# Optimization experiments

Measured on AMD Instinct MI355X. Metric: run time of the kernel, lower is better.

## Reference

```python
import jax, jax.numpy as jnp
import numpy as np

D = 1024
H = 16

def setup_inputs() -> dict:
    key = jax.random.key(0)
    ks = jax.random.split(key, 5)
    x = jax.random.normal(ks[0], (2, 2048, D), dtype=jnp.float32)
    s = 0.02
    W_attn = jax.random.normal(ks[1], (D, 3 * D), dtype=jnp.float32) * s
    b_attn = jnp.zeros((3 * D,), dtype=jnp.float32)
    W_proj = jax.random.normal(ks[2], (D, D), dtype=jnp.float32) * s
    b_proj = jnp.zeros((D,), dtype=jnp.float32)
    return {"x": x, "W_attn": W_attn, "b_attn": b_attn, "W_proj": W_proj, "b_proj": b_proj}

def reference(x, W_attn, b_attn, W_proj, b_proj):
    B, S, E = x.shape
    hd = E // H  # head dim
    qkv = x @ W_attn + b_attn  # [B,S,3E]
    q, k, v = jnp.split(qkv, 3, axis=-1)
    # [B,S,E] -> [B,H,S,hd]
    q = q.reshape(B, S, H, hd).transpose(0, 2, 1, 3)
    k = k.reshape(B, S, H, hd).transpose(0, 2, 1, 3)
    v = v.reshape(B, S, H, hd).transpose(0, 2, 1, 3)
    att = jnp.einsum('bhqd,bhkd->bhqk', q, k) * (1.0 / jnp.sqrt(jnp.float32(hd)))
    causal = jnp.tril(jnp.ones((S, S), dtype=bool))
    att = jnp.where(causal, att, -jnp.inf)
    att = jax.nn.softmax(att, axis=-1)
    y = jnp.einsum('bhqk,bhkd->bhqd', att, v)
    y = y.transpose(0, 2, 1, 3).reshape(B, S, E)
    return y @ W_proj + b_proj
```

## Files before the change

kernel.cpp:

```cpp
#include <hip/hip_runtime.h>
#include <hip/hip_bf16.h>
#include <stdint.h>


typedef __attribute__((ext_vector_type(4))) float  f32x4;
typedef __attribute__((ext_vector_type(8))) __bf16 bf16x8;
typedef __attribute__((ext_vector_type(4))) short  s16x4;
typedef __attribute__((ext_vector_type(8))) short  s16x8;

#define MFMA(a, b, c) __builtin_amdgcn_mfma_f32_16x16x32_bf16((a), (b), (c), 0, 0, 0)

#if defined(__HIP_DEVICE_COMPILE__)
#define MFMA16(a, b, c) __builtin_amdgcn_mfma_f32_16x16x16bf16_1k((a), (b), (c), 0, 0, 0)
#else
#define MFMA16(a, b, c) (c)
#endif

__device__ __forceinline__ short f2bf(float x) {
#if defined(__HIP_DEVICE_COMPILE__)
  union { __bf16 b; short s; } u; u.b = (__bf16)x; return u.s;
#else
  union { float f; unsigned u; } v; v.f = x;
  unsigned r = v.u + 0x7FFFu + ((v.u >> 16) & 1u);
  return (short)(r >> 16);
#endif
}

__device__ __forceinline__ void gload16(const void* gptr, void* lptr) {
  __builtin_amdgcn_global_load_lds(
      (const __attribute__((address_space(1))) void*)gptr,
      (__attribute__((address_space(3))) void*)lptr, 16, 0, 0);
}


__global__ __launch_bounds__(256) void k_prep(const float* __restrict__ x,
                                              const float* __restrict__ Wa,
                                              const float* __restrict__ Wp,
                                              short* __restrict__ x_bf,
                                              short* __restrict__ Wt_a,
                                              short* __restrict__ Wt_p) {
  __shared__ float tile[32][33];
  const int id = blockIdx.x;
  if (id < 4096) {
    const int i = (id * 256 + threadIdx.x) * 4;
    float4 v = *(const float4*)(x + i);
    s16x4 o;
    o[0] = f2bf(v.x); o[1] = f2bf(v.y); o[2] = f2bf(v.z); o[3] = f2bf(v.w);
    *(s16x4*)(x_bf + i) = o;
    return;
  }
  const float* W; short* Wt; int R, C, bx, by;
  if (id < 7168) {
    const int id2 = id - 4096;
    W = Wa; Wt = Wt_a; R = 1024; C = 3072;
    bx = (id2 % 96) * 32; by = (id2 / 96) * 32;
  } else {
    const int id2 = id - 7168;
    W = Wp; Wt = Wt_p; R = 1024; C = 1024;
    bx = (id2 & 31) * 32; by = (id2 >> 5) * 32;
  }
  const int tx = threadIdx.x & 31, ty = threadIdx.x >> 5;
#pragma unroll
  for (int i = 0; i < 4; ++i)
    tile[ty + i * 8][tx] = W[(long)(by + ty + i * 8) * C + bx + tx];
  __syncthreads();
#pragma unroll
  for (int i = 0; i < 4; ++i)
    Wt[(long)(bx + ty + i * 8) * R + by + tx] = f2bf(tile[tx][ty + i * 8]);
}


template <int EPI>
__global__ __launch_bounds__(256) void k_gemm(const short* __restrict__ A,
                                              const short* __restrict__ Bt,
                                              const float* __restrict__ bias,
                                              int M, int N, int K,
                                              short* __restrict__ q_out,
                                              short* __restrict__ k_out,
                                              short* __restrict__ vt_out,
                                              float* __restrict__ c_out) {
  __shared__ short As[3][4096];
  __shared__ short Bs[3][4096];
  const int tid  = threadIdx.x;
  const int lane = tid & 63;
  const int wave = tid >> 6;
  const int wm = (wave >> 1) * 64, wn = (wave & 1) * 64;
  const int bm = blockIdx.y * 128, bn = blockIdx.x * 128;
  const int v_  = (tid & 7) ^ ((tid >> 3) & 7);
  const int rsw = 2 * (tid >> 3) + (v_ >> 2);
  const int csw = (v_ & 3) * 8;
  const short* Ag = A + (long)(bm + rsw) * K + csw;
  const short* Bg = Bt + (long)(bn + rsw) * K + csw;
  const int fr = lane & 15, fg = lane >> 4;

  f32x4 acc[4][4];
#pragma unroll
  for (int i = 0; i < 4; ++i)
#pragma unroll
    for (int j = 0; j < 4; ++j) acc[i][j] = (f32x4){0.f, 0.f, 0.f, 0.f};

  auto stage = [&](int buf, int kt) {
    gload16(Ag + kt, &As[buf][tid * 8]);
    gload16(Ag + kt + 64 * K, &As[buf][2048 + tid * 8]);
    gload16(Bg + kt, &Bs[buf][tid * 8]);
    gload16(Bg + kt + 64 * K, &Bs[buf][2048 + tid * 8]);
  };
  const int slotA = (((fr & 1) << 2) + fg) ^ ((fr >> 1) & 7);
  auto compute = [&](int buf) {
    bf16x8 af[4], bfr[4];
    const short* Ar = &As[buf][((wm + fr) >> 1) * 64 + slotA * 8];
    const short* Br = &Bs[buf][((wn + fr) >> 1) * 64 + slotA * 8];
#pragma unroll
    for (int mi = 0; mi < 4; ++mi) af[mi] = *(const bf16x8*)(Ar + mi * 512);
#pragma unroll
    for (int ni = 0; ni < 4; ++ni) bfr[ni] = *(const bf16x8*)(Br + ni * 512);
#pragma unroll
    for (int mi = 0; mi < 4; ++mi)
#pragma unroll
      for (int ni = 0; ni < 4; ++ni)
        acc[mi][ni] = MFMA(af[mi], bfr[ni], acc[mi][ni]);
  };

  const int NT = K >> 5;
  stage(0, 0);
  stage(1, 32);
  for (int t = 0; t < NT - 1; ++t) {
    asm volatile("s_waitcnt vmcnt(4)" ::: "memory");
    __builtin_amdgcn_s_barrier();
    asm volatile("" ::: "memory");
    if (t + 2 < NT) stage((t + 2) % 3, (t + 2) << 5);
    compute(t % 3);
  }
  asm volatile("s_waitcnt vmcnt(0)" ::: "memory");
  __builtin_amdgcn_s_barrier();
  asm volatile("" ::: "memory");
  compute((NT - 1) % 3);

  const float QSC = 0.125f * 1.44269504088896341f;
#pragma unroll
  for (int mi = 0; mi < 4; ++mi) {
#pragma unroll
    for (int ni = 0; ni < 4; ++ni) {
      const int gcol  = bn + wn + ni * 16 + fr;
      const float bv  = bias[gcol];
      const int grow0 = bm + wm + mi * 16 + fg * 4;
      if (EPI == 0) {
        const int which = gcol >> 10;
        const int e = gcol & 1023;
        const int h = e >> 6, d = e & 63;
#pragma unroll
        for (int r = 0; r < 4; ++r) {
          const int mrow = grow0 + r;
          const int b = mrow >> 11, s = mrow & 2047;
          const float av = acc[mi][ni][r] + bv;
          if (which == 0)      q_out[((long)(b * 16 + h) * 2048 + s) * 64 + d] = f2bf(av * QSC);
          else if (which == 1) k_out[((long)(b * 16 + h) * 2048 + s) * 64 + d] = f2bf(av);
          else                 vt_out[((long)(b * 16 + h) * 64 + d) * 2048 + s] = f2bf(av);
        }
      } else {
#pragma unroll
        for (int r = 0; r < 4; ++r)
          c_out[(long)(grow0 + r) * N + gcol] = acc[mi][ni][r] + bv;
      }
    }
  }
}


__global__ __launch_bounds__(256, 4) void k_attn(const short* __restrict__ Qb,
                                                 const short* __restrict__ Kb,
                                                 const short* __restrict__ Vt,
                                                 short* __restrict__ Y) {
  __shared__ short smem[2][2][4096];
  const int bh = blockIdx.x;
  const int strip = 31 - blockIdx.y;
  const int qw0 = strip * 64;
  const int b = bh >> 4, h = bh & 15;
  const int tid = threadIdx.x;
  const int w = tid >> 6, lane = tid & 63;
  const int ql = lane & 15, g = lane >> 4;
  const short* Kp = Kb + (long)bh * 2048 * 64;
  const short* Vp = Vt + (long)bh * 64 * 2048;
  const short* Qp = Qb + ((long)bh * 2048 + qw0 + w * 16) * 64;

  const bf16x8 qf0 = *(const bf16x8*)(Qp + ql * 64 + g * 8);
  const bf16x8 qf1 = *(const bf16x8*)(Qp + ql * 64 + 32 + g * 8);

  const int sr_ = tid >> 3, sj_ = tid & 7;

  s16x4 ones;
  ones[0] = ones[1] = ones[2] = ones[3] = (short)0x3F80;

  f32x4 o[4];
#pragma unroll
  for (int df = 0; df < 4; ++df) o[df] = (f32x4){0.f, 0.f, 0.f, 0.f};
  f32x4 o_l = (f32x4){0.f, 0.f, 0.f, 0.f};
  const int nt = strip + 1;

  {
#pragma unroll
    for (int j = 0; j < 2; ++j) {
      const int r = j * 32 + sr_;
      const int c = sj_ ^ (r & 7);
      gload16(Kp + (long)r * 64 + c * 8, &smem[0][0][j * 2048 + tid * 8]);
      gload16(Vp + (long)r * 2048 + c * 8, &smem[0][1][j * 2048 + tid * 8]);
    }
  }

  for (int t = 0; t < nt; ++t) {
    const int cur = t & 1;
    __syncthreads();
    if (t + 1 < nt) {
      const int k0n = (t + 1) * 64;
#pragma unroll
      for (int j = 0; j < 2; ++j) {
        const int r = j * 32 + sr_;
        const int c = sj_ ^ (r & 7);
        gload16(Kp + (long)(k0n + r) * 64 + c * 8, &smem[cur ^ 1][0][j * 2048 + tid * 8]);
        gload16(Vp + (long)r * 2048 + k0n + c * 8, &smem[cur ^ 1][1][j * 2048 + tid * 8]);
      }
    }
    const short* Kl = &smem[cur][0][0];
    const short* Vl = &smem[cur][1][0];
    const bool diag = (t == strip);

    float z[16];
    __builtin_amdgcn_s_setprio(1);
#pragma unroll
    for (int kf = 0; kf < 4; ++kf) {
      if (!diag || kf <= w) {
        const int r = kf * 16 + ql;
        const bf16x8 ka = *(const bf16x8*)(Kl + r * 64 + ((g ^ (r & 7)) * 8));
        const bf16x8 kb = *(const bf16x8*)(Kl + r * 64 + (((4 + g) ^ (r & 7)) * 8));
        f32x4 zz = (f32x4){0.f, 0.f, 0.f, 0.f};
        zz = MFMA(ka, qf0, zz);
        zz = MFMA(kb, qf1, zz);
        if (diag && kf == w) {
#pragma unroll
          for (int r4 = 0; r4 < 4; ++r4)
            z[kf * 4 + r4] = (g * 4 + r4 <= ql) ? zz[r4] : -3.0e38f;
        } else {
#pragma unroll
          for (int r4 = 0; r4 < 4; ++r4) z[kf * 4 + r4] = zz[r4];
        }
      } else {
#pragma unroll
        for (int r4 = 0; r4 < 4; ++r4) z[kf * 4 + r4] = -3.0e38f;
      }
    }
    __builtin_amdgcn_s_setprio(0);

    __builtin_amdgcn_s_setprio(1);
#pragma unroll
    for (int kf = 0; kf < 4; ++kf) {
      if (!diag || kf <= w) {
        s16x4 pk;
        pk[0] = f2bf(exp2f(z[kf * 4 + 0]));
        pk[1] = f2bf(exp2f(z[kf * 4 + 1]));
        pk[2] = f2bf(exp2f(z[kf * 4 + 2]));
        pk[3] = f2bf(exp2f(z[kf * 4 + 3]));
        o_l = MFMA16(ones, pk, o_l);
#pragma unroll
        for (int df = 0; df < 4; ++df) {
          const int d = df * 16 + ql;
          const int c = kf * 2 + (g >> 1);
          const s16x4 vk = *(const s16x4*)(Vl + d * 64 + ((c ^ (d & 7)) * 8) + (g & 1) * 4);
          o[df] = MFMA16(vk, pk, o[df]);
        }
      }
    }
    __builtin_amdgcn_s_setprio(0);
  }

  __syncthreads();
  float* ot = (float*)&smem[0][0][0] + w * 1040;
  const float linv = 1.f / o_l[0];
#pragma unroll
  for (int df = 0; df < 4; ++df)
#pragma unroll
    for (int r = 0; r < 4; ++r)
      ot[ql * 65 + df * 16 + g * 4 + r] = o[df][r] * linv;
  const int q2 = lane >> 2, c4 = (lane & 3) * 16;
  short* Yp = Y + ((long)(b * 2048 + qw0 + w * 16 + q2)) * 1024 + h * 64 + c4;
  s16x8 y0, y1;
#pragma unroll
  for (int j = 0; j < 8; ++j) {
    y0[j] = f2bf(ot[q2 * 65 + c4 + j]);
    y1[j] = f2bf(ot[q2 * 65 + c4 + 8 + j]);
  }
  *(s16x8*)Yp = y0;
  *((s16x8*)(Yp + 8)) = y1;
}


extern "C" void kernel_launch(void* const* d_in, const int* in_sizes, int n_in,
                              void* d_out, int out_size, void* d_ws, size_t ws_size,
                              hipStream_t stream) {
  const float* x      = (const float*)d_in[0];
  const float* W_attn = (const float*)d_in[1];
  const float* b_attn = (const float*)d_in[2];
  const float* W_proj = (const float*)d_in[3];
  const float* b_proj = (const float*)d_in[4];
  float* out = (float*)d_out;

  char* ws = (char*)d_ws;
  short* x_bf = (short*)(ws);
  short* Wt_a = (short*)(ws + 8388608);
  short* Wt_p = (short*)(ws + 14680064);
  short* Qb   = (short*)(ws + 16777216);
  short* Kb   = (short*)(ws + 25165824);
  short* Vtb  = (short*)(ws + 33554432);
  short* y_bf = (short*)(ws + 41943040);

  k_prep<<<8192, 256, 0, stream>>>(x, W_attn, W_proj, x_bf, Wt_a, Wt_p);
  k_gemm<0><<<dim3(24, 32), 256, 0, stream>>>(x_bf, Wt_a, b_attn, 4096, 3072, 1024,
                                              Qb, Kb, Vtb, nullptr);
  k_attn<<<dim3(32, 32), 256, 0, stream>>>(Qb, Kb, Vtb, y_bf);
  k_gemm<1><<<dim3(8, 32), 256, 0, stream>>>(y_bf, Wt_p, b_proj, 4096, 1024, 1024,
                                             nullptr, nullptr, nullptr, out);
}
```

Before: 116.5 us.

## Stage V-transpose epilogue through LDS and swizzle block order for XCD locality

```diff
diff --git a/kernel.cpp b/kernel.cpp
--- a/kernel.cpp
+++ b/kernel.cpp
@@ -79,13 +79,22 @@
                                               short* __restrict__ k_out,
                                               short* __restrict__ vt_out,
                                               float* __restrict__ c_out) {
-  __shared__ short As[3][4096];
-  __shared__ short Bs[3][4096];
+  __shared__ short LDSbuf[24576];
+  short* As = LDSbuf;
+  short* Bs = LDSbuf + 12288;
   const int tid  = threadIdx.x;
   const int lane = tid & 63;
   const int wave = tid >> 6;
   const int wm = (wave >> 1) * 64, wn = (wave & 1) * 64;
-  const int bm = blockIdx.y * 128, bn = blockIdx.x * 128;
+  int bxi, byi;
+  if (EPI == 0) {
+    const int orig = blockIdx.y * 24 + blockIdx.x;
+    const int swz = (orig & 7) * 96 + (orig >> 3);
+    bxi = swz % 24; byi = swz / 24;
+  } else {
+    bxi = blockIdx.x; byi = blockIdx.y;
+  }
+  const int bm = byi * 128, bn = bxi * 128;
   const int v_  = (tid & 7) ^ ((tid >> 3) & 7);
   const int rsw = 2 * (tid >> 3) + (v_ >> 2);
   const int csw = (v_ & 3) * 8;
@@ -100,16 +109,16 @@
     for (int j = 0; j < 4; ++j) acc[i][j] = (f32x4){0.f, 0.f, 0.f, 0.f};
 
   auto stage = [&](int buf, int kt) {
-    gload16(Ag + kt, &As[buf][tid * 8]);
-    gload16(Ag + kt + 64 * K, &As[buf][2048 + tid * 8]);
-    gload16(Bg + kt, &Bs[buf][tid * 8]);
-    gload16(Bg + kt + 64 * K, &Bs[buf][2048 + tid * 8]);
+    gload16(Ag + kt, &As[buf * 4096 + tid * 8]);
+    gload16(Ag + kt + 64 * K, &As[buf * 4096 + 2048 + tid * 8]);
+    gload16(Bg + kt, &Bs[buf * 4096 + tid * 8]);
+    gload16(Bg + kt + 64 * K, &Bs[buf * 4096 + 2048 + tid * 8]);
   };
   const int slotA = (((fr & 1) << 2) + fg) ^ ((fr >> 1) & 7);
   auto compute = [&](int buf) {
     bf16x8 af[4], bfr[4];
-    const short* Ar = &As[buf][((wm + fr) >> 1) * 64 + slotA * 8];
-    const short* Br = &Bs[buf][((wn + fr) >> 1) * 64 + slotA * 8];
+    const short* Ar = &As[buf * 4096 + ((wm + fr) >> 1) * 64 + slotA * 8];
+    const short* Br = &Bs[buf * 4096 + ((wn + fr) >> 1) * 64 + slotA * 8];
 #pragma unroll
     for (int mi = 0; mi < 4; ++mi) af[mi] = *(const bf16x8*)(Ar + mi * 512);
 #pragma unroll
@@ -137,30 +146,59 @@
   compute((NT - 1) % 3);
 
   const float QSC = 0.125f * 1.44269504088896341f;
-#pragma unroll
-  for (int mi = 0; mi < 4; ++mi) {
-#pragma unroll
-    for (int ni = 0; ni < 4; ++ni) {
-      const int gcol  = bn + wn + ni * 16 + fr;
-      const float bv  = bias[gcol];
-      const int grow0 = bm + wm + mi * 16 + fg * 4;
-      if (EPI == 0) {
-        const int which = gcol >> 10;
-        const int e = gcol & 1023;
-        const int h = e >> 6, d = e & 63;
-#pragma unroll
-        for (int r = 0; r < 4; ++r) {
-          const int mrow = grow0 + r;
-          const int b = mrow >> 11, s = mrow & 2047;
-          const float av = acc[mi][ni][r] + bv;
-          if (which == 0)      q_out[((long)(b * 16 + h) * 2048 + s) * 64 + d] = f2bf(av * QSC);
-          else if (which == 1) k_out[((long)(b * 16 + h) * 2048 + s) * 64 + d] = f2bf(av);
-          else                 vt_out[((long)(b * 16 + h) * 64 + d) * 2048 + s] = f2bf(av);
+  const int whichB = (EPI == 0) ? (bn >> 10) : 0;
+
+  if (EPI == 0 && whichB == 2) {
+    __syncthreads();
+#pragma unroll
+    for (int mi = 0; mi < 4; ++mi) {
+#pragma unroll
+      for (int ni = 0; ni < 4; ++ni) {
+        const int cc = wn + ni * 16 + fr;
+        const float bv = bias[bn + cc];
+        const int rr = wm + mi * 16 + fg * 4;
+        s16x4 pv;
+#pragma unroll
+        for (int r = 0; r < 4; ++r) pv[r] = f2bf(acc[mi][ni][r] + bv);
+        *(s16x4*)&LDSbuf[cc * 136 + rr] = pv;
+      }
+    }
+    __syncthreads();
+    const int bV = bm >> 11, sBase = bm & 2047;
+    const int h0v = (bn & 1023) >> 6;
+    const int c2 = tid >> 1, hf = tid & 1;
+    const int h2 = h0v + (c2 >> 6), d2 = c2 & 63;
+    short* dst = vt_out + ((long)(bV * 16 + h2) * 64 + d2) * 2048 + sBase + hf * 64;
+    const short* src = &LDSbuf[c2 * 136 + hf * 64];
+#pragma unroll
+    for (int j = 0; j < 8; ++j)
+      *(s16x8*)(dst + j * 8) = *(const s16x8*)(src + j * 8);
+  } else {
+#pragma unroll
+    for (int mi = 0; mi < 4; ++mi) {
+#pragma unroll
+      for (int ni = 0; ni < 4; ++ni) {
+        const int gcol  = bn + wn + ni * 16 + fr;
+        const float bv  = bias[gcol];
+        const int grow0 = bm + wm + mi * 16 + fg * 4;
+        if (EPI == 0) {
+          const int e = gcol & 1023;
+          const int h = e >> 6, d = e & 63;
+#pragma unroll
+          for (int r = 0; r < 4; ++r) {
+            const int mrow = grow0 + r;
+            const int b = mrow >> 11, s = mrow & 2047;
+            const float av = acc[mi][ni][r] + bv;
+            if (whichB == 0)
+              q_out[((long)(b * 16 + h) * 2048 + s) * 64 + d] = f2bf(av * QSC);
+            else
+              k_out[((long)(b * 16 + h) * 2048 + s) * 64 + d] = f2bf(av);
+          }
+        } else {
+#pragma unroll
+          for (int r = 0; r < 4; ++r)
+            c_out[(long)(grow0 + r) * N + gcol] = acc[mi][ni][r] + bv;
         }
-      } else {
-#pragma unroll
-        for (int r = 0; r < 4; ++r)
-          c_out[(long)(grow0 + r) * N + gcol] = acc[mi][ni][r] + bv;
       }
     }
   }
@@ -172,8 +210,10 @@
                                                  const short* __restrict__ Vt,
                                                  short* __restrict__ Y) {
   __shared__ short smem[2][2][4096];
-  const int bh = blockIdx.x;
-  const int strip = 31 - blockIdx.y;
+  const int orig = blockIdx.y * 32 + blockIdx.x;
+  const int swz = (orig & 7) * 128 + (orig >> 3);
+  const int bh = swz >> 5;
+  const int strip = 31 - (swz & 31);
   const int qw0 = strip * 64;
   const int b = bh >> 4, h = bh & 15;
   const int tid = threadIdx.x;
```

New measurement: 131.4 us. +12.8%, slower.
